# Kernel tuning notes

Hardware: AMD Instinct MI355X
Metric: run time of the kernel (lower is better)

## Reference

```python
import jax, jax.numpy as jnp
import numpy as np

B, H, W, C = 32, 32, 32, 256
AD, RR = 8, 16
DN = ('NHWC', 'HWIO', 'NHWC')


def _conv(a, w, dil=1, groups=1):
    return jax.lax.conv_general_dilated(a, w, (1, 1), 'SAME', rhs_dilation=(dil, dil),
                                        dimension_numbers=DN, feature_group_count=groups)


def _branch(a, w1, b1, dw, pw, b3, wd, bd):
    # (Conv1x1 + SeparableConv3x3 + DilatedConv3x3), each sigmoid-activated, averaged
    y1 = jax.nn.sigmoid(_conv(a, w1) + b1)
    y3 = jax.nn.sigmoid(_conv(_conv(a, dw, groups=a.shape[-1]), pw) + b3)  # depthwise (no bias) -> pointwise
    yd = jax.nn.sigmoid(_conv(a, wd, dil=2) + bd)
    return (y1 + y3 + yd) / 3.0


def setup_inputs() -> dict:
    key = jax.random.key(0)
    ks = iter(jax.random.split(key, 64))
    nrm = lambda shape, s=0.05: jax.random.normal(next(ks), shape, jnp.float32) * s
    d = {'x': jax.random.normal(next(ks), (B, H, W, C), jnp.float32)}
    for p in ('cc', 'ch', 'cw'):
        d[p + '1_w'] = nrm((1, 1, C, 1)); d[p + '1_b'] = jnp.zeros((1,), jnp.float32)
        d[p + '3_dw'] = nrm((3, 3, 1, C)); d[p + '3_pw'] = nrm((1, 1, C, 1)); d[p + '3_b'] = jnp.zeros((1,), jnp.float32)
        d[p + 'd_w'] = nrm((3, 3, C, 1)); d[p + 'd_b'] = jnp.zeros((1,), jnp.float32)
    d['branch_w'] = jax.random.uniform(next(ks), (3,), jnp.float32, -0.05, 0.05)
    d['d1_w'] = nrm((C, RR)); d['d1_b'] = jnp.zeros((RR,), jnp.float32)
    d['d2_w'] = nrm((RR, 1)); d['d2_b'] = jnp.zeros((1,), jnp.float32)
    for p in ('q', 'k', 'v'):
        d[p + '_w'] = nrm((1, 1, 3, AD)); d[p + '_b'] = jnp.zeros((AD,), jnp.float32)
    d['o_w'] = nrm((1, 1, AD, 1)); d['o_b'] = jnp.zeros((1,), jnp.float32)
    d['gamma'] = jnp.ones((H, W, C), jnp.float32)
    d['beta'] = jnp.zeros((H, W, C), jnp.float32)
    return d


def reference(x, cc1_w, cc1_b, cc3_dw, cc3_pw, cc3_b, ccd_w, ccd_b,
              ch1_w, ch1_b, ch3_dw, ch3_pw, ch3_b, chd_w, chd_b,
              cw1_w, cw1_b, cw3_dw, cw3_pw, cw3_b, cwd_w, cwd_b,
              branch_w, d1_w, d1_b, d2_w, d2_b,
              q_w, q_b, k_w, k_b, v_w, v_b, o_w, o_b, gamma, beta):
    Bx, Hx, Wx, Cx = x.shape
    # global SE context: GAP -> Dense(relu) -> Dense(sigmoid) -> broadcast over H,W
    g = jnp.mean(x, axis=(1, 2), keepdims=True)                       # [B,1,1,C]
    g = jax.nn.relu(g @ d1_w + d1_b)
    g = jax.nn.sigmoid(g @ d2_w + d2_b)                               # [B,1,1,1]
    # channel branch: mean over H,W -> convs over [B,1,1,C] -> scalar gate
    ca = _branch(jnp.mean(x, axis=(1, 2), keepdims=True), cc1_w, cc1_b, cc3_dw, cc3_pw, cc3_b, ccd_w, ccd_b)  # [B,1,1,1]
    x_c = x * ca
    # height branch: mean over W -> [B,1,H,C] -> convs -> [B,1,H,1] -> gate per-H
    ha_in = jnp.transpose(jnp.mean(x, axis=2, keepdims=True), (0, 2, 1, 3))
    ha = _branch(ha_in, ch1_w, ch1_b, ch3_dw, ch3_pw, ch3_b, chd_w, chd_b)
    x_h = x * jnp.transpose(ha, (0, 2, 1, 3))                         # [B,H,1,1] broadcast
    # width branch: mean over H -> [B,1,W,C] -> convs -> [B,1,W,1] -> gate per-W
    wa = _branch(jnp.mean(x, axis=1, keepdims=True), cw1_w, cw1_b, cw3_dw, cw3_pw, cw3_b, cwd_w, cwd_b)
    x_w = x * wa
    bw = jax.nn.softmax(branch_w)
    combined = bw[0] * x_c + bw[1] * x_h + bw[2] * x_w
    # small self-attention over the 3 channel-mean maps
    maps = jnp.concatenate([jnp.mean(x_c, axis=-1, keepdims=True),
                            jnp.mean(x_h, axis=-1, keepdims=True),
                            jnp.mean(x_w, axis=-1, keepdims=True)], axis=-1)  # [B,H,W,3]
    Q = (jnp.einsum('bhwc,co->bhwo', maps, q_w[0, 0]) + q_b).reshape(Bx, Hx * Wx, AD)
    K = (jnp.einsum('bhwc,co->bhwo', maps, k_w[0, 0]) + k_b).reshape(Bx, Hx * Wx, AD)
    V = (jnp.einsum('bhwc,co->bhwo', maps, v_w[0, 0]) + v_b).reshape(Bx, Hx * Wx, AD)
    att = jax.nn.softmax(jnp.einsum('bnd,bmd->bnm', Q, K) / jnp.sqrt(jnp.float32(AD)), axis=-1)
    ao = jnp.einsum('bnm,bmd->bnd', att, V).reshape(Bx, Hx, Wx, AD)
    cross = jax.nn.sigmoid(jnp.einsum('bhwd,do->bhwo', ao, o_w[0, 0]) + o_b)  # [B,H,W,1]
    y = combined * cross * g + x
    # LayerNorm over (H,W,C) per sample, keras eps=1e-3
    mu = jnp.mean(y, axis=(1, 2, 3), keepdims=True)
    var = jnp.mean((y - mu) ** 2, axis=(1, 2, 3), keepdims=True)
    return (y - mu) / jnp.sqrt(var + 1e-3) * gamma + beta
```

## Files before the change

### kernel.cpp

```cpp
#include <hip/hip_runtime.h>


#define B_   32
#define H_   32
#define W_   32
#define C_   256
#define N_   1024
#define HWC_ (32*32*256)

#define OFF_XW    0
#define OFF_XH    262144
#define OFF_MC    524288
#define OFF_M2    557056
#define OFF_T     589824
#define OFF_HA    622592
#define OFF_WA    623616
#define OFF_CA    624640
#define OFF_G     624672
#define OFF_CST   624704
#define OFF_LNP   624736
#define WS_FLOATS 628832

#if __has_builtin(__builtin_amdgcn_exp2f)
#define EXP2F(x) __builtin_amdgcn_exp2f(x)
#else
#define EXP2F(x) exp2f(x)
#endif

__device__ __forceinline__ float sigm_(float v){ return 1.f/(1.f + __expf(-v)); }
__device__ __forceinline__ float dot4_(float4 a, float4 b){
  return a.x*b.x + a.y*b.y + a.z*b.z + a.w*b.w;
}

__global__ __launch_bounds__(256) void kAB(const float* __restrict__ x, float* __restrict__ ws){
  __shared__ float4 sl4[256];
  const int blk = blockIdx.x;
  const int tid = threadIdx.x, lane = tid & 63, wv = tid >> 6;
  if (blk < 1024){
    const int b = blk >> 5, h = blk & 31;
    const float* xp = x + (size_t)(b*H_ + h)*(W_*C_);
    float4 v[8];
    #pragma unroll
    for (int k = 0; k < 8; ++k) v[k] = ((const float4*)xp)[tid + k*256];
    #pragma unroll
    for (int k = 0; k < 8; ++k){
      float s = v[k].x + v[k].y + v[k].z + v[k].w;
      float q = v[k].x*v[k].x + v[k].y*v[k].y + v[k].z*v[k].z + v[k].w*v[k].w;
      #pragma unroll
      for (int d = 1; d < 64; d <<= 1){ s += __shfl_xor(s, d); q += __shfl_xor(q, d); }
      if (lane == 0){
        const int w = k*4 + wv;
        ws[OFF_MC + b*N_ + h*W_ + w] = s * (1.f/C_);
        ws[OFF_M2 + b*N_ + h*W_ + w] = q;
      }
    }
    float4 a = v[0];
    #pragma unroll
    for (int k = 1; k < 8; ++k){ a.x += v[k].x; a.y += v[k].y; a.z += v[k].z; a.w += v[k].w; }
    sl4[tid] = a;
    __syncthreads();
    if (tid < 64){
      const float4 p0 = sl4[tid], p1 = sl4[tid+64], p2 = sl4[tid+128], p3 = sl4[tid+192];
      float4 o;
      o.x = (p0.x+p1.x+p2.x+p3.x)*(1.f/W_);
      o.y = (p0.y+p1.y+p2.y+p3.y)*(1.f/W_);
      o.z = (p0.z+p1.z+p2.z+p3.z)*(1.f/W_);
      o.w = (p0.w+p1.w+p2.w+p3.w)*(1.f/W_);
      ((float4*)(ws + OFF_XW + (b*H_ + h)*C_))[tid] = o;
    }
  } else {
    const int blk2 = blk - 1024, b = blk2 >> 5, w = blk2 & 31;
    const int hh = tid >> 6, c4 = (tid & 63)*4;
    const float* xp = x + (size_t)b*HWC_ + (size_t)w*C_ + c4;
    float4 acc = {0.f,0.f,0.f,0.f};
    #pragma unroll
    for (int hb = 0; hb < 8; ++hb){
      const int h = hb*4 + hh;
      const float4 v = *(const float4*)(xp + (size_t)h*(W_*C_));
      acc.x += v.x; acc.y += v.y; acc.z += v.z; acc.w += v.w;
    }
    sl4[tid] = acc;
    __syncthreads();
    if (tid < 64){
      const float4 a = sl4[tid], b2 = sl4[tid+64], c = sl4[tid+128], d = sl4[tid+192];
      float4 o;
      o.x = (a.x+b2.x+c.x+d.x)*(1.f/H_);
      o.y = (a.y+b2.y+c.y+d.y)*(1.f/H_);
      o.z = (a.z+b2.z+c.z+d.z)*(1.f/H_);
      o.w = (a.w+b2.w+c.w+d.w)*(1.f/H_);
      *(float4*)&ws[OFF_XH + (b*W_ + w)*C_ + tid*4] = o;
    }
  }
}

__global__ __launch_bounds__(256) void kC(float* __restrict__ ws,
  const float* __restrict__ cc1_w, const float* __restrict__ cc1_b, const float* __restrict__ cc3_dw,
  const float* __restrict__ cc3_pw, const float* __restrict__ cc3_b, const float* __restrict__ ccd_w, const float* __restrict__ ccd_b,
  const float* __restrict__ ch1_w, const float* __restrict__ ch1_b, const float* __restrict__ ch3_dw,
  const float* __restrict__ ch3_pw, const float* __restrict__ ch3_b, const float* __restrict__ chd_w, const float* __restrict__ chd_b,
  const float* __restrict__ cw1_w, const float* __restrict__ cw1_b, const float* __restrict__ cw3_dw,
  const float* __restrict__ cw3_pw, const float* __restrict__ cw3_b, const float* __restrict__ cwd_w, const float* __restrict__ cwd_b,
  const float* __restrict__ branch_w, const float* __restrict__ d1_w, const float* __restrict__ d1_b,
  const float* __restrict__ d2_w, const float* __restrict__ d2_b,
  const float* __restrict__ q_w, const float* __restrict__ q_b, const float* __restrict__ k_w, const float* __restrict__ k_b,
  const float* __restrict__ v_w, const float* __restrict__ v_b, const float* __restrict__ o_w, const float* __restrict__ o_b)
{
  const int b = blockIdx.x, y = blockIdx.y;
  const int tid = threadIdx.x, lane = tid & 63, wv = tid >> 6;

  if (y < 16){
    const int prof = y >> 3;
    const int h = ((y & 7) << 2) | wv;
    const float* P  = ws + (prof ? OFF_XH : OFF_XW) + b*(32*C_);
    const float* w1 = prof ? cw1_w  : ch1_w;
    const float* b1 = prof ? cw1_b  : ch1_b;
    const float* dw = prof ? cw3_dw : ch3_dw;
    const float* pw = prof ? cw3_pw : ch3_pw;
    const float* b3 = prof ? cw3_b  : ch3_b;
    const float* wd = prof ? cwd_w  : chd_w;
    const float* bd = prof ? cwd_b  : chd_b;
    const int c4 = lane*4;
    const float4 z4 = {0.f,0.f,0.f,0.f};
    const float4 r0  = *(const float4*)(P + h*C_ + c4);
    const float4 rm1 = (h > 0)  ? *(const float4*)(P + (h-1)*C_ + c4) : z4;
    const float4 rp1 = (h < 31) ? *(const float4*)(P + (h+1)*C_ + c4) : z4;
    const float4 rm2 = (h > 1)  ? *(const float4*)(P + (h-2)*C_ + c4) : z4;
    const float4 rp2 = (h < 30) ? *(const float4*)(P + (h+2)*C_ + c4) : z4;
    const float4 w1q = *(const float4*)(w1 + c4);
    const float4 d3  = *(const float4*)(dw + 3*C_ + c4);
    const float4 d4  = *(const float4*)(dw + 4*C_ + c4);
    const float4 d5  = *(const float4*)(dw + 5*C_ + c4);
    const float4 pwq = *(const float4*)(pw + c4);
    const float4 g3  = *(const float4*)(wd + 3*C_ + c4);
    const float4 g4  = *(const float4*)(wd + 4*C_ + c4);
    const float4 g5  = *(const float4*)(wd + 5*C_ + c4);
    float s1 = dot4_(r0, w1q);
    float4 dv;
    dv.x = rm1.x*d3.x + r0.x*d4.x + rp1.x*d5.x;
    dv.y = rm1.y*d3.y + r0.y*d4.y + rp1.y*d5.y;
    dv.z = rm1.z*d3.z + r0.z*d4.z + rp1.z*d5.z;
    dv.w = rm1.w*d3.w + r0.w*d4.w + rp1.w*d5.w;
    float s3 = dot4_(dv, pwq);
    float sd = (rm2.x*g3.x + r0.x*g4.x + rp2.x*g5.x)
             + (rm2.y*g3.y + r0.y*g4.y + rp2.y*g5.y)
             + (rm2.z*g3.z + r0.z*g4.z + rp2.z*g5.z)
             + (rm2.w*g3.w + r0.w*g4.w + rp2.w*g5.w);
    #pragma unroll
    for (int d = 1; d < 64; d <<= 1){ s1 += __shfl_xor(s1,d); s3 += __shfl_xor(s3,d); sd += __shfl_xor(sd,d); }
    if (lane == 0)
      ws[(prof ? OFF_WA : OFF_HA) + b*32 + h] =
          (sigm_(s1 + b1[0]) + sigm_(s3 + b3[0]) + sigm_(sd + bd[0])) * (1.f/3.f);
    return;
  }

  __shared__ float gvec[C_];
  { float s = 0.f;
    const float* P = ws + OFF_XW + b*(32*C_);
    #pragma unroll
    for (int h = 0; h < H_; ++h) s += P[h*C_ + tid];
    gvec[tid] = s * (1.f/H_); }
  __syncthreads();

  if (wv == 0){
    float s1 = 0.f, s3 = 0.f, sd = 0.f;
    #pragma unroll
    for (int k = 0; k < 4; ++k){
      const int c = lane + k*64;
      const float v = gvec[c];
      s1 = fmaf(v, cc1_w[c], s1);
      s3 = fmaf(v*cc3_dw[4*C_+c], cc3_pw[c], s3);
      sd = fmaf(v, ccd_w[4*C_+c], sd);
    }
    #pragma unroll
    for (int d = 1; d < 64; d <<= 1){ s1 += __shfl_xor(s1,d); s3 += __shfl_xor(s3,d); sd += __shfl_xor(sd,d); }
    if (lane == 0)
      ws[OFF_CA + b] = (sigm_(s1+cc1_b[0]) + sigm_(s3+cc3_b[0]) + sigm_(sd+ccd_b[0])) * (1.f/3.f);
  } else if (wv == 1){
    const int r16 = lane & 15, cg = lane >> 4;
    float s = 0.f;
    #pragma unroll
    for (int i = 0; i < 64; ++i){
      const int c = cg*64 + i;
      s = fmaf(gvec[c], d1_w[c*16 + r16], s);
    }
    s += __shfl_xor(s, 16); s += __shfl_xor(s, 32);
    float t = fmaxf(s + d1_b[r16], 0.f) * d2_w[r16];
    t += __shfl_xor(t, 1); t += __shfl_xor(t, 2); t += __shfl_xor(t, 4); t += __shfl_xor(t, 8);
    if (lane == 0) ws[OFF_G + b] = sigm_(t + d2_b[0]);
  } else if (wv == 2 && b == 0){
    if (lane < 16){
      const int i = lane >> 2, j = lane & 3;
      float s = 0.f;
      #pragma unroll
      for (int d = 0; d < 8; ++d){
        const float qv = (i < 3) ? q_w[i*8+d] : q_b[d];
        const float kv = (j < 3) ? k_w[j*8+d] : k_b[d];
        s = fmaf(qv, kv, s);
      }
      ws[OFF_CST + i*4 + j] = s * 0.51010305898f;
    } else if (lane < 19){
      const int i = lane - 16;
      float s = 0.f;
      #pragma unroll
      for (int d = 0; d < 8; ++d) s = fmaf(v_w[i*8+d], o_w[d], s);
      ws[OFF_CST + lane] = s;
    } else if (lane == 19){
      float s = o_b[0];
      #pragma unroll
      for (int d = 0; d < 8; ++d) s = fmaf(v_b[d], o_w[d], s);
      ws[OFF_CST + 19] = s;
    } else if (lane == 20){
      const float b0 = branch_w[0], b1 = branch_w[1], b2 = branch_w[2];
      const float mx = fmaxf(b0, fmaxf(b1, b2));
      const float e0 = __expf(b0-mx), e1 = __expf(b1-mx), e2 = __expf(b2-mx);
      const float inv = 1.f/(e0+e1+e2);
      ws[OFF_CST+20] = e0*inv; ws[OFF_CST+21] = e1*inv; ws[OFF_CST+22] = e2*inv;
      ws[OFF_CST+23] = 0.f;
    }
  }
}

__global__ __launch_bounds__(256, 4) void kD(float* __restrict__ ws){
  __shared__ __align__(16) float mcs[N_];
  __shared__ __align__(16) float qs [N_];
  __shared__ float ha_s[32], wa_s[32], cst[24], sc[2], red[8];
  const int blk = blockIdx.x, b = blk >> 6, rblk = blk & 63;
  const int tid = threadIdx.x, lane = tid & 63, wv = tid >> 6;
  const int r = tid >> 4, sub = tid & 15;
  const int sh = sub >> 3, sw = sub & 7;
  const int n = rblk*16 + r;
  const int hn = n >> 5, wn = n & 31;

  const float4 v  = ((const float4*)(ws + OFF_MC + b*N_))[tid];
  const float m2v = ws[OFF_M2 + b*N_ + n];
  const float mcn = ws[OFF_MC + b*N_ + n];
  if (tid < 32){ ha_s[tid] = ws[OFF_HA + b*32 + tid]; wa_s[tid] = ws[OFF_WA + b*32 + tid]; }
  else if (tid >= 64 && tid < 88) cst[tid-64] = ws[OFF_CST + (tid-64)];
  else if (tid == 96){ sc[0] = ws[OFF_CA + b]; sc[1] = ws[OFF_G + b]; }
  *(float4*)&mcs[tid*4] = v;
  __syncthreads();

  const float ca = sc[0], gg = sc[1];
  {
    const int hm0 = tid >> 3;
    const int wm0 = (tid*4) & 31;
    const float base = ca*cst[16] + cst[17]*ha_s[hm0];
    float4 q;
    q.x = v.x * (base + cst[18]*wa_s[wm0+0]);
    q.y = v.y * (base + cst[18]*wa_s[wm0+1]);
    q.z = v.z * (base + cst[18]*wa_s[wm0+2]);
    q.w = v.w * (base + cst[18]*wa_s[wm0+3]);
    *(float4*)&qs[tid*4] = q;
  }
  __syncthreads();

  const float u0 = mcn*ca, u1 = mcn*ha_s[hn], u2 = mcn*wa_s[wn];
  const float p0 = u0*cst[0] + u1*cst[4] + u2*cst[8]  + cst[12];
  const float p1 = u0*cst[1] + u1*cst[5] + u2*cst[9]  + cst[13];
  const float p2 = u0*cst[2] + u1*cst[6] + u2*cst[10] + cst[14];
  const float p3 = u0*cst[3] + u1*cst[7] + u2*cst[11] + cst[15];
  const float pc = p0 * ca;

  const float4 w4 = *(const float4*)&wa_s[4*sw];
  float4 pw;
  pw.x = p2*w4.x; pw.y = p2*w4.y; pw.z = p2*w4.z; pw.w = p2*w4.w;

  float Z = 0.f, ACC = 0.f;
  #pragma unroll
  for (int i = 0; i < 16; ++i){
    const int hm = sh*16 + i;
    const float th = fmaf(p1, ha_s[hm], pc);
    const float4 m4 = *(const float4*)&mcs[hm*32 + 4*sw];
    const float4 q4 = *(const float4*)&qs [hm*32 + 4*sw];
    { const float ee = EXP2F(fmaf(m4.x, th + pw.x, p3)); Z += ee; ACC = fmaf(ee, q4.x, ACC); }
    { const float ee = EXP2F(fmaf(m4.y, th + pw.y, p3)); Z += ee; ACC = fmaf(ee, q4.y, ACC); }
    { const float ee = EXP2F(fmaf(m4.z, th + pw.z, p3)); Z += ee; ACC = fmaf(ee, q4.z, ACC); }
    { const float ee = EXP2F(fmaf(m4.w, th + pw.w, p3)); Z += ee; ACC = fmaf(ee, q4.w, ACC); }
  }
  #pragma unroll
  for (int d = 1; d < 16; d <<= 1){
    Z   += __shfl_xor(Z, d);
    ACC += __shfl_xor(ACC, d);
  }

  float t1 = 0.f, t2 = 0.f;
  if (sub == 0){
    const float dot = ACC / Z + cst[19];
    const float cross = 1.f / (1.f + __expf(-dot));
    const float S = cst[20]*ca + cst[21]*ha_s[hn] + cst[22]*wa_s[wn];
    const float T = fmaf(S*cross, gg, 1.f);
    ws[OFF_T + b*N_ + n] = T;
    t1 = T * mcn * (float)C_;
    t2 = T * T * m2v;
  }
  #pragma unroll
  for (int d = 1; d < 64; d <<= 1){ t1 += __shfl_xor(t1,d); t2 += __shfl_xor(t2,d); }
  if (lane == 0){ red[wv] = t1; red[4+wv] = t2; }
  __syncthreads();
  if (tid == 0){
    ws[OFF_LNP + (b*64 + rblk)*2 + 0] = red[0]+red[1]+red[2]+red[3];
    ws[OFF_LNP + (b*64 + rblk)*2 + 1] = red[4]+red[5]+red[6]+red[7];
  }
}

__global__ __launch_bounds__(256) void kF(const float* __restrict__ x, const float* __restrict__ gamma,
                                          const float* __restrict__ beta, const float* __restrict__ ws,
                                          float* __restrict__ out){
  const int blk = blockIdx.x, b = blk >> 5, h = blk & 31;
  const int tid = threadIdx.x;
  __shared__ float a1s[32];
  __shared__ float mu_r[2];
  if (tid < 64){
    float s1 = ws[OFF_LNP + (b*64 + tid)*2 + 0];
    float s2 = ws[OFF_LNP + (b*64 + tid)*2 + 1];
    #pragma unroll
    for (int d = 1; d < 64; d <<= 1){ s1 += __shfl_xor(s1, d); s2 += __shfl_xor(s2, d); }
    if (tid == 0){
      const float mu  = s1 * (1.f/HWC_);
      const float var = s2 * (1.f/HWC_) - mu*mu;
      const float rstd = rsqrtf(var + 1e-3f);
      mu_r[0] = mu * rstd; mu_r[1] = rstd;
    }
  }
  __syncthreads();
  if (tid < 32) a1s[tid] = ws[OFF_T + b*N_ + h*32 + tid] * mu_r[1];
  __syncthreads();
  const float murstd = mu_r[0];
  const size_t base = (size_t)(b*H_ + h)*(W_*C_);
  const float4* xp = (const float4*)(x + base);
  const float4* gp = (const float4*)(gamma + (size_t)h*(W_*C_));
  const float4* bp = (const float4*)(beta  + (size_t)h*(W_*C_));
  float4* op = (float4*)(out + base);
  #pragma unroll
  for (int k = 0; k < 8; ++k){
    const int f = tid + k*256;
    const float a1 = a1s[f >> 6];
    const float4 xv = xp[f], gv = gp[f], bv = bp[f];
    float4 o;
    o.x = fmaf(fmaf(xv.x, a1, -murstd), gv.x, bv.x);
    o.y = fmaf(fmaf(xv.y, a1, -murstd), gv.y, bv.y);
    o.z = fmaf(fmaf(xv.z, a1, -murstd), gv.z, bv.z);
    o.w = fmaf(fmaf(xv.w, a1, -murstd), gv.w, bv.w);
    op[f] = o;
  }
}

extern "C" void kernel_launch(void* const* d_in, const int* in_sizes, int n_in,
                              void* d_out, int out_size, void* d_ws, size_t ws_size,
                              hipStream_t stream){
  (void)in_sizes; (void)n_in; (void)out_size;
  if (ws_size < (size_t)WS_FLOATS * sizeof(float)) return;
  const float* x      = (const float*)d_in[0];
  const float* cc1_w  = (const float*)d_in[1];
  const float* cc1_b  = (const float*)d_in[2];
  const float* cc3_dw = (const float*)d_in[3];
  const float* cc3_pw = (const float*)d_in[4];
  const float* cc3_b  = (const float*)d_in[5];
  const float* ccd_w  = (const float*)d_in[6];
  const float* ccd_b  = (const float*)d_in[7];
  const float* ch1_w  = (const float*)d_in[8];
  const float* ch1_b  = (const float*)d_in[9];
  const float* ch3_dw = (const float*)d_in[10];
  const float* ch3_pw = (const float*)d_in[11];
  const float* ch3_b  = (const float*)d_in[12];
  const float* chd_w  = (const float*)d_in[13];
  const float* chd_b  = (const float*)d_in[14];
  const float* cw1_w  = (const float*)d_in[15];
  const float* cw1_b  = (const float*)d_in[16];
  const float* cw3_dw = (const float*)d_in[17];
  const float* cw3_pw = (const float*)d_in[18];
  const float* cw3_b  = (const float*)d_in[19];
  const float* cwd_w  = (const float*)d_in[20];
  const float* cwd_b  = (const float*)d_in[21];
  const float* branch_w = (const float*)d_in[22];
  const float* d1_w   = (const float*)d_in[23];
  const float* d1_b   = (const float*)d_in[24];
  const float* d2_w   = (const float*)d_in[25];
  const float* d2_b   = (const float*)d_in[26];
  const float* q_w    = (const float*)d_in[27];
  const float* q_b    = (const float*)d_in[28];
  const float* k_w    = (const float*)d_in[29];
  const float* k_b    = (const float*)d_in[30];
  const float* v_w    = (const float*)d_in[31];
  const float* v_b    = (const float*)d_in[32];
  const float* o_w    = (const float*)d_in[33];
  const float* o_b    = (const float*)d_in[34];
  const float* gamma  = (const float*)d_in[35];
  const float* beta   = (const float*)d_in[36];
  float* ws = (float*)d_ws;
  float* out = (float*)d_out;

  kAB<<<dim3(2048), dim3(256), 0, stream>>>(x, ws);
  kC<<<dim3(B_, 17), dim3(256), 0, stream>>>(ws,
      cc1_w, cc1_b, cc3_dw, cc3_pw, cc3_b, ccd_w, ccd_b,
      ch1_w, ch1_b, ch3_dw, ch3_pw, ch3_b, chd_w, chd_b,
      cw1_w, cw1_b, cw3_dw, cw3_pw, cw3_b, cwd_w, cwd_b,
      branch_w, d1_w, d1_b, d2_w, d2_b,
      q_w, q_b, k_w, k_b, v_w, v_b, o_w, o_b);
  kD<<<dim3(B_*64), dim3(256), 0, stream>>>(ws);
  kF<<<dim3(B_*H_), dim3(256), 0, stream>>>(x, gamma, beta, ws, out);
}
```

Measured before the change: 42.67 us.

## Fold profile convolutions into per-row partial dot products inside the stats pass

The first kernel now handles only the per-(b,h) row blocks. It computes the W-profile and H-profile convolution taps as channel dot products directly from the already-loaded rows, using linearity of the mean. This removes the second 1024-block pass that re-read x column-wise to build the H-mean profile, and it shrinks the context kernel to one block per sample that only sums small partials and applies the shifted stencil. The cost is extra shuffle reductions (seven per row chunk) in the bandwidth-bound pass, plus changed floating-point summation order.

Measured after the change: 54.55 us. 1.28x slower.

```diff
diff --git a/kernel.cpp b/kernel.cpp
--- a/kernel.cpp
+++ b/kernel.cpp
@@ -8,8 +8,9 @@
 #define N_   1024
 #define HWC_ (32*32*256)
 
-#define OFF_XW    0
-#define OFF_XH    262144
+#define OFF_TWP   0
+#define OFF_TH    262144
+#define OFF_CGP   270336
 #define OFF_MC    524288
 #define OFF_M2    557056
 #define OFF_T     589824
@@ -27,167 +28,195 @@
 #define EXP2F(x) exp2f(x)
 #endif
 
+#define RED6(X) { X += __shfl_xor(X,1); X += __shfl_xor(X,2); X += __shfl_xor(X,4); \
+                  X += __shfl_xor(X,8); X += __shfl_xor(X,16); X += __shfl_xor(X,32); }
+
 __device__ __forceinline__ float sigm_(float v){ return 1.f/(1.f + __expf(-v)); }
 __device__ __forceinline__ float dot4_(float4 a, float4 b){
   return a.x*b.x + a.y*b.y + a.z*b.z + a.w*b.w;
 }
-
-__global__ __launch_bounds__(256) void kAB(const float* __restrict__ x, float* __restrict__ ws){
+__device__ __forceinline__ float4 mul4_(float4 a, float4 b){
+  float4 r; r.x=a.x*b.x; r.y=a.y*b.y; r.z=a.z*b.z; r.w=a.w*b.w; return r;
+}
+
+__global__ __launch_bounds__(256) void kAB(const float* __restrict__ x, float* __restrict__ ws,
+    const float* __restrict__ ch1_w, const float* __restrict__ ch3_dw, const float* __restrict__ ch3_pw,
+    const float* __restrict__ chd_w,
+    const float* __restrict__ cw1_w, const float* __restrict__ cw3_dw, const float* __restrict__ cw3_pw,
+    const float* __restrict__ cwd_w,
+    const float* __restrict__ cc1_w, const float* __restrict__ cc3_dw, const float* __restrict__ cc3_pw,
+    const float* __restrict__ ccd_w, const float* __restrict__ d1_w)
+{
   __shared__ float4 sl4[256];
-  const int blk = blockIdx.x;
+  const int blk = blockIdx.x, b = blk >> 5, h = blk & 31;
   const int tid = threadIdx.x, lane = tid & 63, wv = tid >> 6;
-  if (blk < 1024){
-    const int b = blk >> 5, h = blk & 31;
-    const float* xp = x + (size_t)(b*H_ + h)*(W_*C_);
-    float4 v[8];
-    #pragma unroll
-    for (int k = 0; k < 8; ++k) v[k] = ((const float4*)xp)[tid + k*256];
+  const int c4 = lane*4;
+  const float* xp = x + (size_t)blk*(W_*C_);
+  float4 v[8];
+  #pragma unroll
+  for (int k = 0; k < 8; ++k) v[k] = ((const float4*)xp)[tid + k*256];
+
+  #pragma unroll
+  for (int k = 0; k < 8; ++k){
+    float s = v[k].x + v[k].y + v[k].z + v[k].w;
+    float q = v[k].x*v[k].x + v[k].y*v[k].y + v[k].z*v[k].z + v[k].w*v[k].w;
+    RED6(s); RED6(q);
+    if (lane == 0){
+      const int w = k*4 + wv;
+      ws[OFF_MC + b*N_ + h*W_ + w] = s * (1.f/C_);
+      ws[OFF_M2 + b*N_ + h*W_ + w] = q;
+    }
+  }
+
+  {
+    const float4 pwq = *(const float4*)(cw3_pw + c4);
+    const float4 wq0 = *(const float4*)(cw1_w + c4);
+    const float4 wq1 = mul4_(*(const float4*)(cw3_dw + 3*C_ + c4), pwq);
+    const float4 wq2 = mul4_(*(const float4*)(cw3_dw + 4*C_ + c4), pwq);
+    const float4 wq3 = mul4_(*(const float4*)(cw3_dw + 5*C_ + c4), pwq);
+    const float4 wq4 = *(const float4*)(cwd_w + 3*C_ + c4);
+    const float4 wq5 = *(const float4*)(cwd_w + 4*C_ + c4);
+    const float4 wq6 = *(const float4*)(cwd_w + 5*C_ + c4);
     #pragma unroll
     for (int k = 0; k < 8; ++k){
-      float s = v[k].x + v[k].y + v[k].z + v[k].w;
-      float q = v[k].x*v[k].x + v[k].y*v[k].y + v[k].z*v[k].z + v[k].w*v[k].w;
-      #pragma unroll
-      for (int d = 1; d < 64; d <<= 1){ s += __shfl_xor(s, d); q += __shfl_xor(q, d); }
+      const int w = k*4 + wv;
+      float d0 = dot4_(v[k], wq0), d1 = dot4_(v[k], wq1), d2 = dot4_(v[k], wq2);
+      float d3 = dot4_(v[k], wq3), d4 = dot4_(v[k], wq4), d5 = dot4_(v[k], wq5);
+      float d6 = dot4_(v[k], wq6);
+      RED6(d0); RED6(d1); RED6(d2); RED6(d3); RED6(d4); RED6(d5); RED6(d6);
       if (lane == 0){
-        const int w = k*4 + wv;
-        ws[OFF_MC + b*N_ + h*W_ + w] = s * (1.f/C_);
-        ws[OFF_M2 + b*N_ + h*W_ + w] = q;
+        const float sc = 1.f/32.f;
+        float4 o1; o1.x = d0*sc; o1.y = d1*sc; o1.z = d2*sc; o1.w = d3*sc;
+        float4 o2; o2.x = d4*sc; o2.y = d5*sc; o2.z = d6*sc; o2.w = 0.f;
+        *(float4*)&ws[OFF_TWP + (size_t)blk*256 + w*8]     = o1;
+        *(float4*)&ws[OFF_TWP + (size_t)blk*256 + w*8 + 4] = o2;
       }
     }
+  }
+
+  {
     float4 a = v[0];
     #pragma unroll
     for (int k = 1; k < 8; ++k){ a.x += v[k].x; a.y += v[k].y; a.z += v[k].z; a.w += v[k].w; }
     sl4[tid] = a;
-    __syncthreads();
-    if (tid < 64){
-      const float4 p0 = sl4[tid], p1 = sl4[tid+64], p2 = sl4[tid+128], p3 = sl4[tid+192];
-      float4 o;
-      o.x = (p0.x+p1.x+p2.x+p3.x)*(1.f/W_);
-      o.y = (p0.y+p1.y+p2.y+p3.y)*(1.f/W_);
-      o.z = (p0.z+p1.z+p2.z+p3.z)*(1.f/W_);
-      o.w = (p0.w+p1.w+p2.w+p3.w)*(1.f/W_);
-      ((float4*)(ws + OFF_XW + (b*H_ + h)*C_))[tid] = o;
+  }
+  __syncthreads();
+  float4 xwq;
+  {
+    const float4 p0 = sl4[lane], p1 = sl4[64+lane], p2 = sl4[128+lane], p3 = sl4[192+lane];
+    xwq.x = p0.x+p1.x+p2.x+p3.x; xwq.y = p0.y+p1.y+p2.y+p3.y;
+    xwq.z = p0.z+p1.z+p2.z+p3.z; xwq.w = p0.w+p1.w+p2.w+p3.w;
+  }
+
+  if (wv == 0){
+    const float4 pwq = *(const float4*)(ch3_pw + c4);
+    const float4 q0 = *(const float4*)(ch1_w + c4);
+    const float4 q1 = mul4_(*(const float4*)(ch3_dw + 3*C_ + c4), pwq);
+    const float4 q2 = mul4_(*(const float4*)(ch3_dw + 4*C_ + c4), pwq);
+    const float4 q3 = mul4_(*(const float4*)(ch3_dw + 5*C_ + c4), pwq);
+    const float4 q4 = *(const float4*)(chd_w + 3*C_ + c4);
+    const float4 q5 = *(const float4*)(chd_w + 4*C_ + c4);
+    const float4 q6 = *(const float4*)(chd_w + 5*C_ + c4);
+    float t0 = dot4_(xwq,q0), t1 = dot4_(xwq,q1), t2 = dot4_(xwq,q2), t3 = dot4_(xwq,q3);
+    float t4 = dot4_(xwq,q4), t5 = dot4_(xwq,q5), t6 = dot4_(xwq,q6);
+    RED6(t0); RED6(t1); RED6(t2); RED6(t3); RED6(t4); RED6(t5); RED6(t6);
+    if (lane == 0){
+      const float sc = 1.f/32.f;
+      float4 o1; o1.x = t0*sc; o1.y = t1*sc; o1.z = t2*sc; o1.w = t3*sc;
+      float4 o2; o2.x = t4*sc; o2.y = t5*sc; o2.z = t6*sc; o2.w = 0.f;
+      *(float4*)&ws[OFF_TH + (size_t)blk*8]     = o1;
+      *(float4*)&ws[OFF_TH + (size_t)blk*8 + 4] = o2;
+    }
+  } else if (wv == 1 || wv == 2){
+    const int rb = (wv == 1) ? 0 : 8;
+    float s[8];
+    #pragma unroll
+    for (int r = 0; r < 8; ++r){
+      s[r] = xwq.x * d1_w[(c4+0)*16 + rb + r]
+           + xwq.y * d1_w[(c4+1)*16 + rb + r]
+           + xwq.z * d1_w[(c4+2)*16 + rb + r]
+           + xwq.w * d1_w[(c4+3)*16 + rb + r];
+      RED6(s[r]);
+    }
+    if (lane == 0){
+      const float sc = 1.f/1024.f;
+      float4 o1; o1.x = s[0]*sc; o1.y = s[1]*sc; o1.z = s[2]*sc; o1.w = s[3]*sc;
+      float4 o2; o2.x = s[4]*sc; o2.y = s[5]*sc; o2.z = s[6]*sc; o2.w = s[7]*sc;
+      *(float4*)&ws[OFF_CGP + (size_t)blk*24 + 8 + (rb)]     = o1;
+      *(float4*)&ws[OFF_CGP + (size_t)blk*24 + 8 + (rb) + 4] = o2;
     }
   } else {
-    const int blk2 = blk - 1024, b = blk2 >> 5, w = blk2 & 31;
-    const int hh = tid >> 6, c4 = (tid & 63)*4;
-    const float* xp = x + (size_t)b*HWC_ + (size_t)w*C_ + c4;
-    float4 acc = {0.f,0.f,0.f,0.f};
-    #pragma unroll
-    for (int hb = 0; hb < 8; ++hb){
-      const int h = hb*4 + hh;
-      const float4 v = *(const float4*)(xp + (size_t)h*(W_*C_));
-      acc.x += v.x; acc.y += v.y; acc.z += v.z; acc.w += v.w;
-    }
-    sl4[tid] = acc;
-    __syncthreads();
-    if (tid < 64){
-      const float4 a = sl4[tid], b2 = sl4[tid+64], c = sl4[tid+128], d = sl4[tid+192];
-      float4 o;
-      o.x = (a.x+b2.x+c.x+d.x)*(1.f/H_);
-      o.y = (a.y+b2.y+c.y+d.y)*(1.f/H_);
-      o.z = (a.z+b2.z+c.z+d.z)*(1.f/H_);
-      o.w = (a.w+b2.w+c.w+d.w)*(1.f/H_);
-      *(float4*)&ws[OFF_XH + (b*W_ + w)*C_ + tid*4] = o;
+    const float4 q0 = *(const float4*)(cc1_w + c4);
+    const float4 q1 = mul4_(*(const float4*)(cc3_dw + 4*C_ + c4), *(const float4*)(cc3_pw + c4));
+    const float4 q2 = *(const float4*)(ccd_w + 4*C_ + c4);
+    float s0 = dot4_(xwq,q0), s1 = dot4_(xwq,q1), s2 = dot4_(xwq,q2);
+    RED6(s0); RED6(s1); RED6(s2);
+    if (lane == 0){
+      const float sc = 1.f/1024.f;
+      float4 o1; o1.x = s0*sc; o1.y = s1*sc; o1.z = s2*sc; o1.w = 0.f;
+      *(float4*)&ws[OFF_CGP + (size_t)blk*24] = o1;
     }
   }
 }
 
 __global__ __launch_bounds__(256) void kC(float* __restrict__ ws,
-  const float* __restrict__ cc1_w, const float* __restrict__ cc1_b, const float* __restrict__ cc3_dw,
-  const float* __restrict__ cc3_pw, const float* __restrict__ cc3_b, const float* __restrict__ ccd_w, const float* __restrict__ ccd_b,
-  const float* __restrict__ ch1_w, const float* __restrict__ ch1_b, const float* __restrict__ ch3_dw,
-  const float* __restrict__ ch3_pw, const float* __restrict__ ch3_b, const float* __restrict__ chd_w, const float* __restrict__ chd_b,
-  const float* __restrict__ cw1_w, const float* __restrict__ cw1_b, const float* __restrict__ cw3_dw,
-  const float* __restrict__ cw3_pw, const float* __restrict__ cw3_b, const float* __restrict__ cwd_w, const float* __restrict__ cwd_b,
-  const float* __restrict__ branch_w, const float* __restrict__ d1_w, const float* __restrict__ d1_b,
+  const float* __restrict__ cc1_b, const float* __restrict__ cc3_b, const float* __restrict__ ccd_b,
+  const float* __restrict__ ch1_b, const float* __restrict__ ch3_b, const float* __restrict__ chd_b,
+  const float* __restrict__ cw1_b, const float* __restrict__ cw3_b, const float* __restrict__ cwd_b,
+  const float* __restrict__ branch_w, const float* __restrict__ d1_b,
   const float* __restrict__ d2_w, const float* __restrict__ d2_b,
-  const float* __restrict__ q_w, const float* __restrict__ q_b, const float* __restrict__ k_w, const float* __restrict__ k_b,
-  const float* __restrict__ v_w, const float* __restrict__ v_b, const float* __restrict__ o_w, const float* __restrict__ o_b)
+  const float* __restrict__ q_w, const float* __restrict__ q_b,
+  const float* __restrict__ k_w, const float* __restrict__ k_b,
+  const float* __restrict__ v_w, const float* __restrict__ v_b,
+  const float* __restrict__ o_w, const float* __restrict__ o_b)
 {
-  const int b = blockIdx.x, y = blockIdx.y;
-  const int tid = threadIdx.x, lane = tid & 63, wv = tid >> 6;
-
-  if (y < 16){
-    const int prof = y >> 3;
-    const int h = ((y & 7) << 2) | wv;
-    const float* P  = ws + (prof ? OFF_XH : OFF_XW) + b*(32*C_);
-    const float* w1 = prof ? cw1_w  : ch1_w;
-    const float* b1 = prof ? cw1_b  : ch1_b;
-    const float* dw = prof ? cw3_dw : ch3_dw;
-    const float* pw = prof ? cw3_pw : ch3_pw;
-    const float* b3 = prof ? cw3_b  : ch3_b;
-    const float* wd = prof ? cwd_w  : chd_w;
-    const float* bd = prof ? cwd_b  : chd_b;
-    const int c4 = lane*4;
-    const float4 z4 = {0.f,0.f,0.f,0.f};
-    const float4 r0  = *(const float4*)(P + h*C_ + c4);
-    const float4 rm1 = (h > 0)  ? *(const float4*)(P + (h-1)*C_ + c4) : z4;
-    const float4 rp1 = (h < 31) ? *(const float4*)(P + (h+1)*C_ + c4) : z4;
-    const float4 rm2 = (h > 1)  ? *(const float4*)(P + (h-2)*C_ + c4) : z4;
-    const float4 rp2 = (h < 30) ? *(const float4*)(P + (h+2)*C_ + c4) : z4;
-    const float4 w1q = *(const float4*)(w1 + c4);
-    const float4 d3  = *(const float4*)(dw + 3*C_ + c4);
-    const float4 d4  = *(const float4*)(dw + 4*C_ + c4);
-    const float4 d5  = *(const float4*)(dw + 5*C_ + c4);
-    const float4 pwq = *(const float4*)(pw + c4);
-    const float4 g3  = *(const float4*)(wd + 3*C_ + c4);
-    const float4 g4  = *(const float4*)(wd + 4*C_ + c4);
-    const float4 g5  = *(const float4*)(wd + 5*C_ + c4);
-    float s1 = dot4_(r0, w1q);
-    float4 dv;
-    dv.x = rm1.x*d3.x + r0.x*d4.x + rp1.x*d5.x;
-    dv.y = rm1.y*d3.y + r0.y*d4.y + rp1.y*d5.y;
-    dv.z = rm1.z*d3.z + r0.z*d4.z + rp1.z*d5.z;
-    dv.w = rm1.w*d3.w + r0.w*d4.w + rp1.w*d5.w;
-    float s3 = dot4_(dv, pwq);
-    float sd = (rm2.x*g3.x + r0.x*g4.x + rp2.x*g5.x)
-             + (rm2.y*g3.y + r0.y*g4.y + rp2.y*g5.y)
-             + (rm2.z*g3.z + r0.z*g4.z + rp2.z*g5.z)
-             + (rm2.w*g3.w + r0.w*g4.w + rp2.w*g5.w);
-    #pragma unroll
-    for (int d = 1; d < 64; d <<= 1){ s1 += __shfl_xor(s1,d); s3 += __shfl_xor(s3,d); sd += __shfl_xor(sd,d); }
-    if (lane == 0)
-      ws[(prof ? OFF_WA : OFF_HA) + b*32 + h] =
-          (sigm_(s1 + b1[0]) + sigm_(s3 + b3[0]) + sigm_(sd + bd[0])) * (1.f/3.f);
-    return;
-  }
-
-  __shared__ float gvec[C_];
-  { float s = 0.f;
-    const float* P = ws + OFF_XW + b*(32*C_);
-    #pragma unroll
-    for (int h = 0; h < H_; ++h) s += P[h*C_ + tid];
-    gvec[tid] = s * (1.f/H_); }
-  __syncthreads();
-
-  if (wv == 0){
-    float s1 = 0.f, s3 = 0.f, sd = 0.f;
-    #pragma unroll
-    for (int k = 0; k < 4; ++k){
-      const int c = lane + k*64;
-      const float v = gvec[c];
-      s1 = fmaf(v, cc1_w[c], s1);
-      s3 = fmaf(v*cc3_dw[4*C_+c], cc3_pw[c], s3);
-      sd = fmaf(v, ccd_w[4*C_+c], sd);
-    }
-    #pragma unroll
-    for (int d = 1; d < 64; d <<= 1){ s1 += __shfl_xor(s1,d); s3 += __shfl_xor(s3,d); sd += __shfl_xor(sd,d); }
-    if (lane == 0)
-      ws[OFF_CA + b] = (sigm_(s1+cc1_b[0]) + sigm_(s3+cc3_b[0]) + sigm_(sd+ccd_b[0])) * (1.f/3.f);
-  } else if (wv == 1){
-    const int r16 = lane & 15, cg = lane >> 4;
-    float s = 0.f;
-    #pragma unroll
-    for (int i = 0; i < 64; ++i){
-      const int c = cg*64 + i;
-      s = fmaf(gvec[c], d1_w[c*16 + r16], s);
-    }
-    s += __shfl_xor(s, 16); s += __shfl_xor(s, 32);
-    float t = fmaxf(s + d1_b[r16], 0.f) * d2_w[r16];
-    t += __shfl_xor(t, 1); t += __shfl_xor(t, 2); t += __shfl_xor(t, 4); t += __shfl_xor(t, 8);
-    if (lane == 0) ws[OFF_G + b] = sigm_(t + d2_b[0]);
-  } else if (wv == 2 && b == 0){
+  __shared__ float red7[32][8];
+  __shared__ float thv [32][8];
+  __shared__ float cg[24];
+  const int b = blockIdx.x, tid = threadIdx.x, lane = tid & 63, wv = tid >> 6;
+
+  {
+    float acc = 0.f;
+    const float* p = ws + OFF_TWP + (size_t)b*8192 + tid;
+    #pragma unroll
+    for (int hh = 0; hh < 32; ++hh) acc += p[hh*256];
+    red7[tid>>3][tid&7] = acc;
+    thv [tid>>3][tid&7] = ws[OFF_TH + (size_t)b*256 + tid];
+  }
+  if (tid < 24){
+    float a = 0.f;
+    #pragma unroll
+    for (int hh = 0; hh < 32; ++hh) a += ws[OFF_CGP + ((size_t)b*32 + hh)*24 + tid];
+    cg[tid] = a;
+  }
+  __syncthreads();
+
+  if (wv == 0 && lane < 32){
+    const int hh = lane;
+    const float s1 = thv[hh][0];
+    const float s3 = thv[hh][2] + (hh>0  ? thv[hh-1][1] : 0.f) + (hh<31 ? thv[hh+1][3] : 0.f);
+    const float sd = thv[hh][5] + (hh>1  ? thv[hh-2][4] : 0.f) + (hh<30 ? thv[hh+2][6] : 0.f);
+    ws[OFF_HA + b*32 + hh] =
+        (sigm_(s1 + ch1_b[0]) + sigm_(s3 + ch3_b[0]) + sigm_(sd + chd_b[0])) * (1.f/3.f);
+  } else if (wv == 1 && lane < 32){
+    const int w = lane;
+    const float s1 = red7[w][0];
+    const float s3 = red7[w][2] + (w>0  ? red7[w-1][1] : 0.f) + (w<31 ? red7[w+1][3] : 0.f);
+    const float sd = red7[w][5] + (w>1  ? red7[w-2][4] : 0.f) + (w<30 ? red7[w+2][6] : 0.f);
+    ws[OFF_WA + b*32 + w] =
+        (sigm_(s1 + cw1_b[0]) + sigm_(s3 + cw3_b[0]) + sigm_(sd + cwd_b[0])) * (1.f/3.f);
+  } else if (wv == 2){
+    if (lane == 0){
+      ws[OFF_CA + b] = (sigm_(cg[0] + cc1_b[0]) + sigm_(cg[1] + cc3_b[0])
+                      + sigm_(cg[2] + ccd_b[0])) * (1.f/3.f);
+    } else if (lane == 1){
+      float acc = d2_b[0];
+      #pragma unroll
+      for (int r = 0; r < 16; ++r)
+        acc = fmaf(fmaxf(cg[8+r] + d1_b[r], 0.f), d2_w[r], acc);
+      ws[OFF_G + b] = sigm_(acc);
+    }
+  } else if (wv == 3 && b == 0){
     if (lane < 16){
       const int i = lane >> 2, j = lane & 3;
       float s = 0.f;
@@ -390,12 +419,13 @@
   float* ws = (float*)d_ws;
   float* out = (float*)d_out;
 
-  kAB<<<dim3(2048), dim3(256), 0, stream>>>(x, ws);
-  kC<<<dim3(B_, 17), dim3(256), 0, stream>>>(ws,
-      cc1_w, cc1_b, cc3_dw, cc3_pw, cc3_b, ccd_w, ccd_b,
-      ch1_w, ch1_b, ch3_dw, ch3_pw, ch3_b, chd_w, chd_b,
-      cw1_w, cw1_b, cw3_dw, cw3_pw, cw3_b, cwd_w, cwd_b,
-      branch_w, d1_w, d1_b, d2_w, d2_b,
+  kAB<<<dim3(1024), dim3(256), 0, stream>>>(x, ws,
+      ch1_w, ch3_dw, ch3_pw, chd_w,
+      cw1_w, cw3_dw, cw3_pw, cwd_w,
+      cc1_w, cc3_dw, cc3_pw, ccd_w, d1_w);
+  kC<<<dim3(B_), dim3(256), 0, stream>>>(ws,
+      cc1_b, cc3_b, ccd_b, ch1_b, ch3_b, chd_b, cw1_b, cw3_b, cwd_b,
+      branch_w, d1_b, d2_w, d2_b,
       q_w, q_b, k_w, k_b, v_w, v_b, o_w, o_b);
   kD<<<dim3(B_*64), dim3(256), 0, stream>>>(ws);
   kF<<<dim3(B_*H_), dim3(256), 0, stream>>>(x, gamma, beta, ws, out);
```
